# Kernel tuning notes

Measured on AMD Instinct MI355X. Metric: run time of the kernel, lower is better.

Reference implementation:

```python
import jax, jax.numpy as jnp
import numpy as np

NOISE_EPS = 1e-2   # Shazeer noisy-gating stddev floor
LN_EPS = 1e-6
LOSS_COEF = 0.01
K = 2              # num_activated_experts


def _layer_norm(x, w, b):
    mu = jnp.mean(x, axis=-1, keepdims=True)
    var = jnp.var(x, axis=-1, keepdims=True)
    return (x - mu) * jax.lax.rsqrt(var + LN_EPS) * w + b


def _cv_squared(v):
    return jnp.var(v) / (jnp.mean(v) ** 2 + 1e-10)


def _normal_cdf(z):
    return 0.5 * (1.0 + jax.scipy.special.erf(z / jnp.sqrt(jnp.asarray(2.0, z.dtype))))


def setup_inputs() -> dict:
    key = jax.random.key(0)
    ks = jax.random.split(key, 8)
    N, D, H, O, E = 8192, 512, 1024, 512, 8
    x = jax.random.normal(ks[0], (N, D), jnp.float32)
    x_offsets = jnp.sort(jax.random.randint(ks[1], (17,), 0, N)).astype(jnp.int64)
    noise = jax.random.normal(ks[2], (N, E), jnp.float32)
    s = 0.02
    return {
        "x": x,
        "x_offsets": x_offsets,
        "max_seq_len": 2048,
        "noise": noise,
        "norm_w": jnp.ones((D,), jnp.float32),
        "norm_bias": jnp.zeros((D,), jnp.float32),
        "w_gate": jax.random.normal(ks[3], (D, E), jnp.float32) * s,
        "w_noise": jax.random.normal(ks[4], (D, E), jnp.float32) * s,
        "W1": jax.random.normal(ks[5], (E, H, D), jnp.float32) * s,  # [E, model_d, input]
        "b1": jnp.zeros((E, H), jnp.float32),
        "W2": jax.random.normal(ks[6], (E, O, H), jnp.float32) * s,  # [E, output, model_d]
        "b2": jnp.zeros((E, O), jnp.float32),
        "output_weight": jax.random.normal(ks[7], (D, O), jnp.float32) * s,
    }


def reference(x, x_offsets, max_seq_len, noise, norm_w, norm_bias, w_gate, w_noise,
              W1, b1, W2, b2, output_weight):
    N, D = x.shape
    E = w_gate.shape[1]
    k_plus = min(K + 1, E)

    # pre-norm
    x_norm = _layer_norm(x, norm_w, norm_bias)

    # noisy top-k gating (training path)
    clean_logits = x_norm @ w_gate                      # [N, E]
    noise_stddev = jax.nn.softplus(x_norm @ w_noise) + NOISE_EPS
    noisy_logits = clean_logits + noise * noise_stddev

    top_logits, top_indices = jax.lax.top_k(noisy_logits, k_plus)   # [N, k+1]
    top_k_logits = top_logits[:, :K]
    top_k_indices = top_indices[:, :K]
    top_k_gates = jax.nn.softmax(top_k_logits, axis=-1)             # [N, K]

    rows = jnp.arange(N)[:, None]
    gates = jnp.zeros((N, E), top_k_gates.dtype).at[rows, top_k_indices].set(top_k_gates)

    # load = prob each expert is in top-k under the gating noise (Shazeer)
    flat = top_logits.reshape(-1)
    pos_in = jnp.arange(N) * k_plus + K
    thr_in = flat[pos_in][:, None]          # (k+1)-th value: threshold if already in
    thr_out = flat[pos_in - 1][:, None]     # k-th value: threshold if currently out
    is_in = noisy_logits > thr_in
    prob_in = _normal_cdf((clean_logits - thr_in) / noise_stddev)
    prob_out = _normal_cdf((clean_logits - thr_out) / noise_stddev)
    load_probs = jnp.where(is_in, prob_in, prob_out)                # [N, E]

    loss = LOSS_COEF * (_cv_squared(gates.sum(0)) + _cv_squared(load_probs.sum(0)))

    # dispatch stats: tokens per expert
    lengths = jnp.zeros((E,), jnp.float32).at[top_k_indices.reshape(-1)].add(1.0)
    load = lengths / lengths.sum()

    # grouped expert MLP (dense one-hot combine; gates are 0 for unrouted experts)
    h = jnp.einsum('nd,ehd->neh', x_norm, W1) + b1                  # [N, E, H]
    a = jax.nn.silu(h)
    y_e = jnp.einsum('neh,eoh->neo', a, W2) + b2                    # [N, E, O]
    y_moe = jnp.einsum('ne,neo->no', gates, y_e)                    # [N, O]

    # shared expert: addmm(y, shared_x=x, output_weight)
    y = y_moe + x @ output_weight
    return y, loss, load
```

## Files before the change

kernel.cpp:

```cpp
#include <hip/hip_runtime.h>
#include <math.h>

typedef unsigned short u16;
typedef unsigned int u32;

#define N_ROWS 8192
#define DDIM 512
#define HDIM 1024
#define ODIM 512
#define NEXP 8
#define MAXPAIRS (N_ROWS * 2)
#define MAXPOS (MAXPAIRS + NEXP * 128)
#define MAXTILES (MAXPOS / 128)

#define SM_CNT 0
#define SM_CUR 8
#define SM_AOFF 16
#define SM_GSUM 32
#define SM_LSUM 40
#define SM_WORDS 64

using short8 = __attribute__((ext_vector_type(8))) short;
using float4v = __attribute__((ext_vector_type(4))) float;

__device__ __forceinline__ u16 f2bf(float f) {
    union { float f; u32 u; } v; v.f = f;
    u32 u = v.u;
    return (u16)((u + 0x7fffu + ((u >> 16) & 1u)) >> 16);
}

__device__ __forceinline__ void async_copy16(u16* lds, const u16* g) {
    __builtin_amdgcn_global_load_lds(
        (const __attribute__((address_space(1))) void*)g,
        (__attribute__((address_space(3))) void*)lds, 16, 0, 0);
}

__global__ __launch_bounds__(512) void init1_kernel(int* small, float* zeropage) {
    int i = threadIdx.x;
    if (i < SM_WORDS) small[i] = 0;
    zeropage[i] = 0.f;
}

#define W1CONV_BLOCKS 4096
#define GATE_BLOCKS 512
__global__ __launch_bounds__(256) void combo_kernel(
    const float* __restrict__ x, const float* __restrict__ noise,
    const float* __restrict__ norm_w, const float* __restrict__ norm_b,
    const float* __restrict__ w_gate, const float* __restrict__ w_noise,
    const float* __restrict__ W1, const float* __restrict__ ow,
    u16* __restrict__ xnorm_bf, u16* __restrict__ x_bf,
    int* __restrict__ pair_expert, float* __restrict__ pair_gate,
    u16* __restrict__ W1b, u16* __restrict__ owT,
    int* __restrict__ small, int* __restrict__ bucket_rows)
{
    __shared__ __align__(16) float sh[NEXP * DDIM * 2 + 64];
    int b = blockIdx.x, tid = threadIdx.x;

    if (b >= GATE_BLOCKS) {
        int cb = b - GATE_BLOCKS;
        if (cb < W1CONV_BLOCKS) {
            size_t i = (size_t)cb * 256 + tid;
            float4 v = ((const float4*)W1)[i];
            ushort4 o;
            o.x = f2bf(v.x); o.y = f2bf(v.y); o.z = f2bf(v.z); o.w = f2bf(v.w);
            ((ushort4*)W1b)[i] = o;
        } else if (cb < W1CONV_BLOCKS + 256) {
            float (*tile)[33] = (float(*)[33])sh;
            int t = cb - W1CONV_BLOCKS;
            int bx = (t & 15) * 32, by = (t >> 4) * 32;
            int tx = tid & 31, ty = tid >> 5;
            for (int r = ty; r < 32; r += 8) tile[r][tx] = ow[(size_t)(by + r) * ODIM + bx + tx];
            __syncthreads();
            for (int r = ty; r < 32; r += 8) owT[(size_t)(bx + r) * DDIM + by + tx] = f2bf(tile[tx][r]);
        } else {
            int i = (cb - W1CONV_BLOCKS - 256) * 256 + tid;
            if (i < MAXPOS) bucket_rows[i] = -1;
        }
        return;
    }

    float* wgT = sh;
    float* wnT = sh + NEXP * DDIM;
    float* blk_g = sh + 2 * NEXP * DDIM;
    float* blk_l = blk_g + NEXP;
    int* blk_c = (int*)(blk_l + NEXP);
    float* smf = (float*)small;

    for (int i = tid; i < NEXP * DDIM; i += 256) {
        int d = i >> 3, e = i & 7;
        wgT[e * DDIM + d] = w_gate[i];
        wnT[e * DDIM + d] = w_noise[i];
    }
    if (tid < NEXP) { blk_g[tid] = 0.f; blk_l[tid] = 0.f; blk_c[tid] = 0; }
    __syncthreads();

    int wave = tid >> 6, lane = tid & 63;
    float nw[8], nb[8];
#pragma unroll
    for (int j = 0; j < 8; j++) { nw[j] = norm_w[j * 64 + lane]; nb[j] = norm_b[j * 64 + lane]; }

    for (int r = 0; r < 4; ++r) {
        int row = b * 16 + wave * 4 + r;
        const float* xr = x + (size_t)row * DDIM;
        float xv[8], s = 0.f, s2 = 0.f;
#pragma unroll
        for (int j = 0; j < 8; j++) { float v = xr[j * 64 + lane]; xv[j] = v; s += v; s2 += v * v; }
#pragma unroll
        for (int o = 32; o; o >>= 1) { s += __shfl_xor(s, o, 64); s2 += __shfl_xor(s2, o, 64); }
        float mu = s * (1.f / DDIM);
        float var = s2 * (1.f / DDIM) - mu * mu;
        float rstd = rsqrtf(var + 1e-6f);

        float acc[16];
#pragma unroll
        for (int e = 0; e < 16; e++) acc[e] = 0.f;
#pragma unroll
        for (int j = 0; j < 8; j++) {
            float v = (xv[j] - mu) * rstd * nw[j] + nb[j];
            int d = j * 64 + lane;
            xnorm_bf[(size_t)row * DDIM + d] = f2bf(v);
            x_bf[(size_t)row * DDIM + d] = f2bf(xv[j]);
#pragma unroll
            for (int e = 0; e < 8; e++) {
                acc[e] += v * wgT[e * DDIM + d];
                acc[8 + e] += v * wnT[e * DDIM + d];
            }
        }
#pragma unroll
        for (int e = 0; e < 16; e++)
#pragma unroll
            for (int o = 32; o; o >>= 1) acc[e] += __shfl_xor(acc[e], o, 64);

        float cl[8], sd[8], nz[8];
#pragma unroll
        for (int e = 0; e < 8; e++) {
            cl[e] = acc[e];
            float t = acc[8 + e];
            float sp = fmaxf(t, 0.f) + log1pf(expf(-fabsf(t)));
            sd[e] = sp + 0.01f;
            nz[e] = cl[e] + noise[(size_t)row * NEXP + e] * sd[e];
        }
        int idx[3]; float val[3]; u32 msk = 0;
#pragma unroll
        for (int t = 0; t < 3; t++) {
            float best = -INFINITY; int bi = 0;
#pragma unroll
            for (int e = 0; e < 8; e++)
                if (!((msk >> e) & 1) && nz[e] > best) { best = nz[e]; bi = e; }
            idx[t] = bi; val[t] = best; msk |= 1u << bi;
        }
        float e1 = expf(val[1] - val[0]);
        float g0 = 1.f / (1.f + e1), g1 = e1 / (1.f + e1);
        float thr_in = val[2], thr_out = val[1];

        if (lane == 0) {
            pair_expert[row * 2] = idx[0]; pair_gate[row * 2] = g0;
            pair_expert[row * 2 + 1] = idx[1]; pair_gate[row * 2 + 1] = g1;
            atomicAdd(&blk_g[idx[0]], g0); atomicAdd(&blk_g[idx[1]], g1);
            atomicAdd(&blk_c[idx[0]], 1); atomicAdd(&blk_c[idx[1]], 1);
#pragma unroll
            for (int e = 0; e < 8; e++) {
                float thr = (nz[e] > thr_in) ? thr_in : thr_out;
                float z = (cl[e] - thr) / sd[e];
                float p = 0.5f * (1.f + erff(z * 0.70710678118654752f));
                atomicAdd(&blk_l[e], p);
            }
        }
    }
    __syncthreads();
    if (tid < NEXP) {
        atomicAdd(smf + SM_GSUM + tid, blk_g[tid]);
        atomicAdd(smf + SM_LSUM + tid, blk_l[tid]);
        atomicAdd(&small[SM_CNT + tid], blk_c[tid]);
    }
}

__global__ __launch_bounds__(256) void scatter_kernel(
    const int* __restrict__ pair_expert, const float* __restrict__ pair_gate,
    int* __restrict__ small, int* __restrict__ bucket_rows, float* __restrict__ gate_by_pos,
    float* __restrict__ out_loss, float* __restrict__ out_load)
{
    __shared__ int aoff[NEXP + 1];
    __shared__ int blk_cnt[NEXP];
    __shared__ int blk_base[NEXP];
    int tid = threadIdx.x;
    if (tid == 0) {
        int acc = 0; aoff[0] = 0;
        for (int e = 0; e < NEXP; e++) { acc += (small[SM_CNT + e] + 127) & ~127; aoff[e + 1] = acc; }
    }
    if (tid < NEXP) blk_cnt[tid] = 0;
    __syncthreads();
    int p = blockIdx.x * 256 + tid;
    int e = pair_expert[p];
    int local = atomicAdd(&blk_cnt[e], 1);
    __syncthreads();
    if (tid < NEXP)
        blk_base[tid] = aoff[tid] + atomicAdd(&small[SM_CUR + tid], blk_cnt[tid]);
    if (blockIdx.x == 0 && tid < NEXP + 1) small[SM_AOFF + tid] = aoff[tid];
    __syncthreads();
    int pos = blk_base[e] + local;
    bucket_rows[pos] = p >> 1;
    gate_by_pos[pos] = pair_gate[p];

    if (blockIdx.x == 0 && tid == 0) {
        const float* gs = (const float*)small + SM_GSUM;
        const float* ls = (const float*)small + SM_LSUM;
        float cv[2];
        for (int t = 0; t < 2; t++) {
            const float* v = t ? ls : gs;
            float m = 0.f;
            for (int k = 0; k < NEXP; k++) m += v[k];
            m *= (1.f / NEXP);
            float var = 0.f;
            for (int k = 0; k < NEXP; k++) { float d = v[k] - m; var += d * d; }
            var *= (1.f / NEXP);
            cv[t] = var / (m * m + 1e-10f);
        }
        out_loss[0] = 0.01f * (cv[0] + cv[1]);
        int tot = 0;
        for (int k = 0; k < NEXP; k++) tot += small[SM_CNT + k];
        float inv = 1.f / (float)tot;
        for (int k = 0; k < NEXP; k++) out_load[k] = (float)small[SM_CNT + k] * inv;
    }
}


__global__ __launch_bounds__(256) void gemmA_kernel(
    const u16* __restrict__ xnorm, const u16* __restrict__ xbf,
    const u16* __restrict__ W1b, const u16* __restrict__ owT,
    const float* __restrict__ W2, u16* __restrict__ W2b,
    const int* __restrict__ bucket_rows, const int* __restrict__ small,
    const float* __restrict__ b1, const u16* __restrict__ zeropage,
    u16* __restrict__ a_buf, float* __restrict__ y)
{
    constexpr int KD = 512;
    __shared__ __align__(16) u16 As[128 * 64];
    __shared__ __align__(16) u16 Bs[128 * 64];

    int tid = threadIdx.x;
    if (blockIdx.y >= 10) {
        int j = (blockIdx.y - 10) * 136 + blockIdx.x;
        if (j >= 2048) return;
        size_t i = (size_t)j * 512 + tid;
#pragma unroll
        for (int t = 0; t < 2; t++, i += 256) {
            float4 v = ((const float4*)W2)[i];
            ushort4 o;
            o.x = f2bf(v.x); o.y = f2bf(v.y); o.z = f2bf(v.z); o.w = f2bf(v.w);
            ((ushort4*)W2b)[i] = o;
        }
        return;
    }

    bool m0 = blockIdx.y < 8;
    int base, bn, e = 0;
    const u16* Bsel;
    if (m0) {
        base = blockIdx.x * 128;
        if (base >= small[SM_AOFF + 8]) return;
        while (e < 7 && base >= small[SM_AOFF + e + 1]) ++e;
        bn = blockIdx.y * 128;
        Bsel = W1b + (size_t)e * HDIM * KD;
    } else {
        int j = (blockIdx.y - 8) * 136 + blockIdx.x;
        if (j >= 256) return;
        base = (j >> 2) * 128;
        bn = (j & 3) * 128;
        Bsel = owT;
    }

    int wave = tid >> 6, lane = tid & 63;
    int lr = lane >> 3;
    int lc = ((lane & 7) ^ lr) * 8;

    const u16* ga[4]; const u16* gb[4];
    u16* la[4]; u16* lb[4];
#pragma unroll
    for (int c = 0; c < 4; c++) {
        int tr = wave * 32 + c * 8;
        if (m0) {
            int r0 = bucket_rows[base + tr + lr];
            ga[c] = ((r0 < 0) ? zeropage : xnorm + (size_t)r0 * KD) + lc;
        } else {
            ga[c] = xbf + (size_t)(base + tr + lr) * KD + lc;
        }
        gb[c] = Bsel + (size_t)(bn + tr + lr) * KD + lc;
        la[c] = &As[tr * 64];
        lb[c] = &Bs[tr * 64];
    }

    int wm = (wave & 1) * 64, wn = (wave >> 1) * 64;
    int fr = lane & 15, kq = lane >> 4, f7 = fr & 7;

    float4v acc[4][4];
#pragma unroll
    for (int i = 0; i < 4; i++)
#pragma unroll
        for (int j = 0; j < 4; j++) acc[i][j] = (float4v){0.f, 0.f, 0.f, 0.f};

    for (int k0 = 0; k0 < KD; k0 += 64) {
        __syncthreads();
#pragma unroll
        for (int c = 0; c < 4; c++) async_copy16(la[c], ga[c] + k0);
#pragma unroll
        for (int c = 0; c < 4; c++) async_copy16(lb[c], gb[c] + k0);
        __syncthreads();
        short8 af[4][2], bf[4][2];
#pragma unroll
        for (int mt = 0; mt < 4; mt++)
#pragma unroll
            for (int kh = 0; kh < 2; kh++)
                af[mt][kh] = *(const short8*)&As[(wm + mt * 16 + fr) * 64 + (((kq + 4 * kh) ^ f7) * 8)];
#pragma unroll
        for (int nt = 0; nt < 4; nt++)
#pragma unroll
            for (int kh = 0; kh < 2; kh++)
                bf[nt][kh] = *(const short8*)&Bs[(wn + nt * 16 + fr) * 64 + (((kq + 4 * kh) ^ f7) * 8)];
#pragma unroll
        for (int mt = 0; mt < 4; mt++)
#pragma unroll
            for (int nt = 0; nt < 4; nt++) {
                acc[mt][nt] = __builtin_amdgcn_mfma_f32_16x16x32_bf16(af[mt][0], bf[nt][0], acc[mt][nt], 0, 0, 0);
                acc[mt][nt] = __builtin_amdgcn_mfma_f32_16x16x32_bf16(af[mt][1], bf[nt][1], acc[mt][nt], 0, 0, 0);
            }
    }

    int rbase = (lane >> 4) * 4, c16 = lane & 15;
#pragma unroll
    for (int nt = 0; nt < 4; nt++) {
        int gn = bn + wn + nt * 16 + c16;
        float bv = m0 ? b1[e * HDIM + gn] : 0.f;
#pragma unroll
        for (int mt = 0; mt < 4; mt++) {
            int gm = base + wm + mt * 16 + rbase;
#pragma unroll
            for (int r = 0; r < 4; r++) {
                float v = acc[mt][nt][r];
                if (m0) {
                    float h = v + bv;
                    float a = h * __builtin_amdgcn_rcpf(1.f + __expf(-h));
                    a_buf[(size_t)(gm + r) * HDIM + gn] = f2bf(a);
                } else {
                    y[(size_t)(gm + r) * ODIM + gn] = v;
                }
            }
        }
    }
}

__global__ __launch_bounds__(256) void gemmB_kernel(
    const u16* __restrict__ a_buf, const u16* __restrict__ W2b,
    const int* __restrict__ bucket_rows, const int* __restrict__ small,
    const float* __restrict__ b2, const float* __restrict__ gate_by_pos,
    float* __restrict__ y)
{
    constexpr int KD = 1024;
    __shared__ __align__(16) u16 As[128 * 32];
    __shared__ __align__(16) u16 Bs[128 * 32];

    int tid = threadIdx.x;
    int base = blockIdx.x * 128;
    if (base >= small[SM_AOFF + 8]) return;
    int e = 0;
    while (e < 7 && base >= small[SM_AOFF + e + 1]) ++e;
    int bn = blockIdx.y * 128;

    int wave = tid >> 6, lane = tid & 63;
    const int trow = wave * 32 + (lane >> 2);
    const int kcol = (lane & 3) * 8;
    const u16* ga0 = a_buf + (size_t)(base + trow) * KD + kcol;
    const u16* ga1 = a_buf + (size_t)(base + trow + 16) * KD + kcol;
    const u16* Bsel = W2b + (size_t)e * ODIM * KD;
    const u16* gb0 = Bsel + (size_t)(bn + trow) * KD + kcol;
    const u16* gb1 = Bsel + (size_t)(bn + trow + 16) * KD + kcol;
    u16* lA0 = &As[(wave * 32) * 32];
    u16* lA1 = &As[(wave * 32 + 16) * 32];
    u16* lB0 = &Bs[(wave * 32) * 32];
    u16* lB1 = &Bs[(wave * 32 + 16) * 32];

    int wm = (wave & 1) * 64, wn = (wave >> 1) * 64;
    int fr = lane & 15, kg = (lane >> 4) * 8;

    float4v acc[4][4];
#pragma unroll
    for (int i = 0; i < 4; i++)
#pragma unroll
        for (int j = 0; j < 4; j++) acc[i][j] = (float4v){0.f, 0.f, 0.f, 0.f};

    for (int k0 = 0; k0 < KD; k0 += 32) {
        __syncthreads();
        async_copy16(lA0, ga0 + k0);
        async_copy16(lA1, ga1 + k0);
        async_copy16(lB0, gb0 + k0);
        async_copy16(lB1, gb1 + k0);
        __syncthreads();
        short8 af[4], bf[4];
#pragma unroll
        for (int mt = 0; mt < 4; mt++) af[mt] = *(const short8*)&As[(wm + mt * 16 + fr) * 32 + kg];
#pragma unroll
        for (int nt = 0; nt < 4; nt++) bf[nt] = *(const short8*)&Bs[(wn + nt * 16 + fr) * 32 + kg];
#pragma unroll
        for (int mt = 0; mt < 4; mt++)
#pragma unroll
            for (int nt = 0; nt < 4; nt++)
                acc[mt][nt] = __builtin_amdgcn_mfma_f32_16x16x32_bf16(af[mt], bf[nt], acc[mt][nt], 0, 0, 0);
    }

    int rbase = (lane >> 4) * 4, c16 = lane & 15;
#pragma unroll
    for (int mt = 0; mt < 4; mt++) {
        int pos0 = base + wm + mt * 16 + rbase;
        int rows[4]; float gs[4];
#pragma unroll
        for (int r = 0; r < 4; r++) { rows[r] = bucket_rows[pos0 + r]; gs[r] = gate_by_pos[pos0 + r]; }
#pragma unroll
        for (int nt = 0; nt < 4; nt++) {
            int gn = bn + wn + nt * 16 + c16;
            float b2v = b2[e * ODIM + gn];
#pragma unroll
            for (int r = 0; r < 4; r++) {
                if (rows[r] >= 0)
                    unsafeAtomicAdd(&y[(size_t)rows[r] * ODIM + gn], gs[r] * (acc[mt][nt][r] + b2v));
            }
        }
    }
}

extern "C" void kernel_launch(void* const* d_in, const int* in_sizes, int n_in,
                              void* d_out, int out_size, void* d_ws, size_t ws_size,
                              hipStream_t stream)
{
    (void)in_sizes; (void)n_in; (void)out_size; (void)ws_size;
    const float* x = (const float*)d_in[0];
    const float* noise = (const float*)d_in[3];
    const float* norm_w = (const float*)d_in[4];
    const float* norm_b = (const float*)d_in[5];
    const float* w_gate = (const float*)d_in[6];
    const float* w_noise = (const float*)d_in[7];
    const float* W1 = (const float*)d_in[8];
    const float* b1 = (const float*)d_in[9];
    const float* W2 = (const float*)d_in[10];
    const float* b2 = (const float*)d_in[11];
    const float* ow = (const float*)d_in[12];

    float* y = (float*)d_out;
    float* out_loss = y + (size_t)N_ROWS * ODIM;
    float* out_load = out_loss + 1;

    char* ws = (char*)d_ws;
    size_t off = 0;
    auto alloc = [&](size_t b) { size_t p = off; off = (off + b + 255) & ~(size_t)255; return p; };
    u16* xnorm_bf = (u16*)(ws + alloc((size_t)N_ROWS * DDIM * 2));
    u16* x_bf     = (u16*)(ws + alloc((size_t)N_ROWS * DDIM * 2));
    u16* W1b      = (u16*)(ws + alloc((size_t)NEXP * HDIM * DDIM * 2));
    u16* W2b      = (u16*)(ws + alloc((size_t)NEXP * ODIM * HDIM * 2));
    u16* owT      = (u16*)(ws + alloc((size_t)DDIM * ODIM * 2));
    u16* a_buf    = (u16*)(ws + alloc((size_t)MAXPOS * HDIM * 2));
    int* pair_expert = (int*)(ws + alloc((size_t)MAXPAIRS * 4));
    float* pair_gate = (float*)(ws + alloc((size_t)MAXPAIRS * 4));
    float* gate_by_pos = (float*)(ws + alloc((size_t)MAXPOS * 4));
    int* bucket_rows = (int*)(ws + alloc((size_t)MAXPOS * 4));
    int* small       = (int*)(ws + alloc(SM_WORDS * 4));
    float* zeropage  = (float*)(ws + alloc(2048));

    init1_kernel<<<1, 512, 0, stream>>>(small, zeropage);
    combo_kernel<<<GATE_BLOCKS + W1CONV_BLOCKS + 256 + 68, 256, 0, stream>>>(
        x, noise, norm_w, norm_b, w_gate, w_noise, W1, ow,
        xnorm_bf, x_bf, pair_expert, pair_gate, W1b, owT, small, bucket_rows);
    scatter_kernel<<<MAXPAIRS / 256, 256, 0, stream>>>(pair_expert, pair_gate, small,
                                                       bucket_rows, gate_by_pos, out_loss, out_load);
    gemmA_kernel<<<dim3(MAXTILES, 10 + 16), 256, 0, stream>>>(xnorm_bf, x_bf, W1b, owT, W2, W2b,
                                                              bucket_rows, small, b1,
                                                              (const u16*)zeropage, a_buf, y);
    gemmB_kernel<<<dim3(MAXTILES, ODIM / 128), 256, 0, stream>>>(a_buf, W2b, bucket_rows, small,
                                                                 b2, gate_by_pos, y);
}
```

Before: 256.2 us.

## Move shared-expert GEMM from gemmA into gemmB with atomic accumulation

The shared-expert x@output_weight GEMM moves out of gemmA and into gemmB as extra blocks. y is now zeroed by new blocks in combo_kernel, and the shared GEMM adds into y atomically instead of storing directly. The aim is to shorten gemmA, which sits on the critical path before gemmB, and let the shared GEMM overlap with the expert down-projection. In exchange it adds a zero-fill pass over y and atomic adds for the shared output, and gemmB now uses the smaller 32-wide K tile for that GEMM.

```diff
diff --git a/kernel.cpp b/kernel.cpp
--- a/kernel.cpp
+++ b/kernel.cpp
@@ -43,6 +43,9 @@
 
 #define W1CONV_BLOCKS 4096
 #define GATE_BLOCKS 512
+#define OWT_BLOCKS 256
+#define BUCKET_BLOCKS 68
+#define YZERO_BLOCKS 1024
 __global__ __launch_bounds__(256) void combo_kernel(
     const float* __restrict__ x, const float* __restrict__ noise,
     const float* __restrict__ norm_w, const float* __restrict__ norm_b,
@@ -51,7 +54,7 @@
     u16* __restrict__ xnorm_bf, u16* __restrict__ x_bf,
     int* __restrict__ pair_expert, float* __restrict__ pair_gate,
     u16* __restrict__ W1b, u16* __restrict__ owT,
-    int* __restrict__ small, int* __restrict__ bucket_rows)
+    int* __restrict__ small, int* __restrict__ bucket_rows, float* __restrict__ y)
 {
     __shared__ __align__(16) float sh[NEXP * DDIM * 2 + 64];
     int b = blockIdx.x, tid = threadIdx.x;
@@ -64,7 +67,7 @@
             ushort4 o;
             o.x = f2bf(v.x); o.y = f2bf(v.y); o.z = f2bf(v.z); o.w = f2bf(v.w);
             ((ushort4*)W1b)[i] = o;
-        } else if (cb < W1CONV_BLOCKS + 256) {
+        } else if (cb < W1CONV_BLOCKS + OWT_BLOCKS) {
             float (*tile)[33] = (float(*)[33])sh;
             int t = cb - W1CONV_BLOCKS;
             int bx = (t & 15) * 32, by = (t >> 4) * 32;
@@ -72,9 +75,15 @@
             for (int r = ty; r < 32; r += 8) tile[r][tx] = ow[(size_t)(by + r) * ODIM + bx + tx];
             __syncthreads();
             for (int r = ty; r < 32; r += 8) owT[(size_t)(bx + r) * DDIM + by + tx] = f2bf(tile[tx][r]);
+        } else if (cb < W1CONV_BLOCKS + OWT_BLOCKS + BUCKET_BLOCKS) {
+            int i = (cb - W1CONV_BLOCKS - OWT_BLOCKS) * 256 + tid;
+            if (i < MAXPOS) bucket_rows[i] = -1;
         } else {
-            int i = (cb - W1CONV_BLOCKS - 256) * 256 + tid;
-            if (i < MAXPOS) bucket_rows[i] = -1;
+            int zb = cb - W1CONV_BLOCKS - OWT_BLOCKS - BUCKET_BLOCKS;
+            size_t i = (size_t)zb * 1024 + tid;
+            float4 zero = {0.f, 0.f, 0.f, 0.f};
+#pragma unroll
+            for (int t = 0; t < 4; t++, i += 256) ((float4*)y)[i] = zero;
         }
         return;
     }
@@ -224,22 +233,20 @@
     }
 }
 
-
 __global__ __launch_bounds__(256) void gemmA_kernel(
-    const u16* __restrict__ xnorm, const u16* __restrict__ xbf,
-    const u16* __restrict__ W1b, const u16* __restrict__ owT,
+    const u16* __restrict__ xnorm, const u16* __restrict__ W1b,
     const float* __restrict__ W2, u16* __restrict__ W2b,
     const int* __restrict__ bucket_rows, const int* __restrict__ small,
     const float* __restrict__ b1, const u16* __restrict__ zeropage,
-    u16* __restrict__ a_buf, float* __restrict__ y)
+    u16* __restrict__ a_buf)
 {
     constexpr int KD = 512;
     __shared__ __align__(16) u16 As[128 * 64];
     __shared__ __align__(16) u16 Bs[128 * 64];
 
     int tid = threadIdx.x;
-    if (blockIdx.y >= 10) {
-        int j = (blockIdx.y - 10) * 136 + blockIdx.x;
+    if (blockIdx.y >= 8) {
+        int j = (blockIdx.y - 8) * 136 + blockIdx.x;
         if (j >= 2048) return;
         size_t i = (size_t)j * 512 + tid;
 #pragma unroll
@@ -252,134 +259,129 @@
         return;
     }
 
-    bool m0 = blockIdx.y < 8;
-    int base, bn, e = 0;
-    const u16* Bsel;
-    if (m0) {
-        base = blockIdx.x * 128;
-        if (base >= small[SM_AOFF + 8]) return;
-        while (e < 7 && base >= small[SM_AOFF + e + 1]) ++e;
-        bn = blockIdx.y * 128;
-        Bsel = W1b + (size_t)e * HDIM * KD;
-    } else {
-        int j = (blockIdx.y - 8) * 136 + blockIdx.x;
-        if (j >= 256) return;
-        base = (j >> 2) * 128;
-        bn = (j & 3) * 128;
-        Bsel = owT;
-    }
-
-    int wave = tid >> 6, lane = tid & 63;
-    int lr = lane >> 3;
-    int lc = ((lane & 7) ^ lr) * 8;
-
-    const u16* ga[4]; const u16* gb[4];
-    u16* la[4]; u16* lb[4];
-#pragma unroll
-    for (int c = 0; c < 4; c++) {
-        int tr = wave * 32 + c * 8;
-        if (m0) {
-            int r0 = bucket_rows[base + tr + lr];
-            ga[c] = ((r0 < 0) ? zeropage : xnorm + (size_t)r0 * KD) + lc;
-        } else {
-            ga[c] = xbf + (size_t)(base + tr + lr) * KD + lc;
-        }
-        gb[c] = Bsel + (size_t)(bn + tr + lr) * KD + lc;
-        la[c] = &As[tr * 64];
-        lb[c] = &Bs[tr * 64];
-    }
-
-    int wm = (wave & 1) * 64, wn = (wave >> 1) * 64;
-    int fr = lane & 15, kq = lane >> 4, f7 = fr & 7;
-
-    float4v acc[4][4];
-#pragma unroll
-    for (int i = 0; i < 4; i++)
-#pragma unroll
-        for (int j = 0; j < 4; j++) acc[i][j] = (float4v){0.f, 0.f, 0.f, 0.f};
-
-    for (int k0 = 0; k0 < KD; k0 += 64) {
-        __syncthreads();
-#pragma unroll
-        for (int c = 0; c < 4; c++) async_copy16(la[c], ga[c] + k0);
-#pragma unroll
-        for (int c = 0; c < 4; c++) async_copy16(lb[c], gb[c] + k0);
-        __syncthreads();
-        short8 af[4][2], bf[4][2];
-#pragma unroll
-        for (int mt = 0; mt < 4; mt++)
-#pragma unroll
-            for (int kh = 0; kh < 2; kh++)
-                af[mt][kh] = *(const short8*)&As[(wm + mt * 16 + fr) * 64 + (((kq + 4 * kh) ^ f7) * 8)];
-#pragma unroll
-        for (int nt = 0; nt < 4; nt++)
-#pragma unroll
-            for (int kh = 0; kh < 2; kh++)
-                bf[nt][kh] = *(const short8*)&Bs[(wn + nt * 16 + fr) * 64 + (((kq + 4 * kh) ^ f7) * 8)];
-#pragma unroll
-        for (int mt = 0; mt < 4; mt++)
-#pragma unroll
-            for (int nt = 0; nt < 4; nt++) {
-                acc[mt][nt] = __builtin_amdgcn_mfma_f32_16x16x32_bf16(af[mt][0], bf[nt][0], acc[mt][nt], 0, 0, 0);
-                acc[mt][nt] = __builtin_amdgcn_mfma_f32_16x16x32_bf16(af[mt][1], bf[nt][1], acc[mt][nt], 0, 0, 0);
-            }
-    }
-
-    int rbase = (lane >> 4) * 4, c16 = lane & 15;
-#pragma unroll
-    for (int nt = 0; nt < 4; nt++) {
-        int gn = bn + wn + nt * 16 + c16;
-        float bv = m0 ? b1[e * HDIM + gn] : 0.f;
-#pragma unroll
-        for (int mt = 0; mt < 4; mt++) {
-            int gm = base + wm + mt * 16 + rbase;
-#pragma unroll
-            for (int r = 0; r < 4; r++) {
-                float v = acc[mt][nt][r];
-                if (m0) {
-                    float h = v + bv;
-                    float a = h * __builtin_amdgcn_rcpf(1.f + __expf(-h));
-                    a_buf[(size_t)(gm + r) * HDIM + gn] = f2bf(a);
-                } else {
-                    y[(size_t)(gm + r) * ODIM + gn] = v;
-                }
-            }
-        }
-    }
-}
-
-__global__ __launch_bounds__(256) void gemmB_kernel(
-    const u16* __restrict__ a_buf, const u16* __restrict__ W2b,
-    const int* __restrict__ bucket_rows, const int* __restrict__ small,
-    const float* __restrict__ b2, const float* __restrict__ gate_by_pos,
-    float* __restrict__ y)
-{
-    constexpr int KD = 1024;
-    __shared__ __align__(16) u16 As[128 * 32];
-    __shared__ __align__(16) u16 Bs[128 * 32];
-
-    int tid = threadIdx.x;
     int base = blockIdx.x * 128;
     if (base >= small[SM_AOFF + 8]) return;
     int e = 0;
     while (e < 7 && base >= small[SM_AOFF + e + 1]) ++e;
     int bn = blockIdx.y * 128;
-
+    const u16* Bsel = W1b + (size_t)e * HDIM * KD;
+
+    int wave = tid >> 6, lane = tid & 63;
+    int lr = lane >> 3;
+    int lc = ((lane & 7) ^ lr) * 8;
+
+    const u16* ga[4]; const u16* gb[4];
+    u16* la[4]; u16* lb[4];
+#pragma unroll
+    for (int c = 0; c < 4; c++) {
+        int tr = wave * 32 + c * 8;
+        int r0 = bucket_rows[base + tr + lr];
+        ga[c] = ((r0 < 0) ? zeropage : xnorm + (size_t)r0 * KD) + lc;
+        gb[c] = Bsel + (size_t)(bn + tr + lr) * KD + lc;
+        la[c] = &As[tr * 64];
+        lb[c] = &Bs[tr * 64];
+    }
+
+    int wm = (wave & 1) * 64, wn = (wave >> 1) * 64;
+    int fr = lane & 15, kq = lane >> 4, f7 = fr & 7;
+
+    float4v acc[4][4];
+#pragma unroll
+    for (int i = 0; i < 4; i++)
+#pragma unroll
+        for (int j = 0; j < 4; j++) acc[i][j] = (float4v){0.f, 0.f, 0.f, 0.f};
+
+    for (int k0 = 0; k0 < KD; k0 += 64) {
+        __syncthreads();
+#pragma unroll
+        for (int c = 0; c < 4; c++) async_copy16(la[c], ga[c] + k0);
+#pragma unroll
+        for (int c = 0; c < 4; c++) async_copy16(lb[c], gb[c] + k0);
+        __syncthreads();
+        short8 af[4][2], bf[4][2];
+#pragma unroll
+        for (int mt = 0; mt < 4; mt++)
+#pragma unroll
+            for (int kh = 0; kh < 2; kh++)
+                af[mt][kh] = *(const short8*)&As[(wm + mt * 16 + fr) * 64 + (((kq + 4 * kh) ^ f7) * 8)];
+#pragma unroll
+        for (int nt = 0; nt < 4; nt++)
+#pragma unroll
+            for (int kh = 0; kh < 2; kh++)
+                bf[nt][kh] = *(const short8*)&Bs[(wn + nt * 16 + fr) * 64 + (((kq + 4 * kh) ^ f7) * 8)];
+#pragma unroll
+        for (int mt = 0; mt < 4; mt++)
+#pragma unroll
+            for (int nt = 0; nt < 4; nt++) {
+                acc[mt][nt] = __builtin_amdgcn_mfma_f32_16x16x32_bf16(af[mt][0], bf[nt][0], acc[mt][nt], 0, 0, 0);
+                acc[mt][nt] = __builtin_amdgcn_mfma_f32_16x16x32_bf16(af[mt][1], bf[nt][1], acc[mt][nt], 0, 0, 0);
+            }
+    }
+
+    int rbase = (lane >> 4) * 4, c16 = lane & 15;
+#pragma unroll
+    for (int nt = 0; nt < 4; nt++) {
+        int gn = bn + wn + nt * 16 + c16;
+        float bv = b1[e * HDIM + gn];
+#pragma unroll
+        for (int mt = 0; mt < 4; mt++) {
+            int gm = base + wm + mt * 16 + rbase;
+#pragma unroll
+            for (int r = 0; r < 4; r++) {
+                float h = acc[mt][nt][r] + bv;
+                float a = h * __builtin_amdgcn_rcpf(1.f + __expf(-h));
+                a_buf[(size_t)(gm + r) * HDIM + gn] = f2bf(a);
+            }
+        }
+    }
+}
+
+__global__ __launch_bounds__(256) void gemmB_kernel(
+    const u16* __restrict__ a_buf, const u16* __restrict__ W2b,
+    const u16* __restrict__ xbf, const u16* __restrict__ owT,
+    const int* __restrict__ bucket_rows, const int* __restrict__ small,
+    const float* __restrict__ b2, const float* __restrict__ gate_by_pos,
+    float* __restrict__ y)
+{
+    __shared__ __align__(16) u16 As[128 * 32];
+    __shared__ __align__(16) u16 Bs[128 * 32];
+
+    int tid = threadIdx.x;
     int wave = tid >> 6, lane = tid & 63;
     const int trow = wave * 32 + (lane >> 2);
     const int kcol = (lane & 3) * 8;
-    const u16* ga0 = a_buf + (size_t)(base + trow) * KD + kcol;
-    const u16* ga1 = a_buf + (size_t)(base + trow + 16) * KD + kcol;
-    const u16* Bsel = W2b + (size_t)e * ODIM * KD;
-    const u16* gb0 = Bsel + (size_t)(bn + trow) * KD + kcol;
-    const u16* gb1 = Bsel + (size_t)(bn + trow + 16) * KD + kcol;
+    int wm = (wave & 1) * 64, wn = (wave >> 1) * 64;
+    int fr = lane & 15, kg = (lane >> 4) * 8;
+
+    bool expertPath = blockIdx.y < 4;
+    int base, bn, e = 0, KD;
+    const u16 *ga0, *ga1, *gb0, *gb1;
+    if (expertPath) {
+        KD = 1024;
+        base = blockIdx.x * 128;
+        if (base >= small[SM_AOFF + 8]) return;
+        while (e < 7 && base >= small[SM_AOFF + e + 1]) ++e;
+        bn = blockIdx.y * 128;
+        ga0 = a_buf + (size_t)(base + trow) * KD + kcol;
+        ga1 = a_buf + (size_t)(base + trow + 16) * KD + kcol;
+        const u16* Bsel = W2b + (size_t)e * ODIM * KD;
+        gb0 = Bsel + (size_t)(bn + trow) * KD + kcol;
+        gb1 = Bsel + (size_t)(bn + trow + 16) * KD + kcol;
+    } else {
+        KD = 512;
+        int j = (blockIdx.y - 4) * 136 + blockIdx.x;
+        if (j >= 256) return;
+        base = (j >> 2) * 128;
+        bn = (j & 3) * 128;
+        ga0 = xbf + (size_t)(base + trow) * KD + kcol;
+        ga1 = xbf + (size_t)(base + trow + 16) * KD + kcol;
+        gb0 = owT + (size_t)(bn + trow) * KD + kcol;
+        gb1 = owT + (size_t)(bn + trow + 16) * KD + kcol;
+    }
     u16* lA0 = &As[(wave * 32) * 32];
     u16* lA1 = &As[(wave * 32 + 16) * 32];
     u16* lB0 = &Bs[(wave * 32) * 32];
     u16* lB1 = &Bs[(wave * 32 + 16) * 32];
-
-    int wm = (wave & 1) * 64, wn = (wave >> 1) * 64;
-    int fr = lane & 15, kg = (lane >> 4) * 8;
 
     float4v acc[4][4];
 #pragma unroll
@@ -407,20 +409,34 @@
     }
 
     int rbase = (lane >> 4) * 4, c16 = lane & 15;
-#pragma unroll
-    for (int mt = 0; mt < 4; mt++) {
-        int pos0 = base + wm + mt * 16 + rbase;
-        int rows[4]; float gs[4];
-#pragma unroll
-        for (int r = 0; r < 4; r++) { rows[r] = bucket_rows[pos0 + r]; gs[r] = gate_by_pos[pos0 + r]; }
-#pragma unroll
-        for (int nt = 0; nt < 4; nt++) {
-            int gn = bn + wn + nt * 16 + c16;
-            float b2v = b2[e * ODIM + gn];
-#pragma unroll
-            for (int r = 0; r < 4; r++) {
-                if (rows[r] >= 0)
-                    unsafeAtomicAdd(&y[(size_t)rows[r] * ODIM + gn], gs[r] * (acc[mt][nt][r] + b2v));
+    if (expertPath) {
+#pragma unroll
+        for (int mt = 0; mt < 4; mt++) {
+            int pos0 = base + wm + mt * 16 + rbase;
+            int rows[4]; float gs[4];
+#pragma unroll
+            for (int r = 0; r < 4; r++) { rows[r] = bucket_rows[pos0 + r]; gs[r] = gate_by_pos[pos0 + r]; }
+#pragma unroll
+            for (int nt = 0; nt < 4; nt++) {
+                int gn = bn + wn + nt * 16 + c16;
+                float b2v = b2[e * ODIM + gn];
+#pragma unroll
+                for (int r = 0; r < 4; r++) {
+                    if (rows[r] >= 0)
+                        unsafeAtomicAdd(&y[(size_t)rows[r] * ODIM + gn], gs[r] * (acc[mt][nt][r] + b2v));
+                }
+            }
+        }
+    } else {
+#pragma unroll
+        for (int mt = 0; mt < 4; mt++) {
+            int gm = base + wm + mt * 16 + rbase;
+#pragma unroll
+            for (int nt = 0; nt < 4; nt++) {
+                int gn = bn + wn + nt * 16 + c16;
+#pragma unroll
+                for (int r = 0; r < 4; r++)
+                    unsafeAtomicAdd(&y[(size_t)(gm + r) * ODIM + gn], acc[mt][nt][r]);
             }
         }
     }
@@ -464,14 +480,15 @@
     float* zeropage  = (float*)(ws + alloc(2048));
 
     init1_kernel<<<1, 512, 0, stream>>>(small, zeropage);
-    combo_kernel<<<GATE_BLOCKS + W1CONV_BLOCKS + 256 + 68, 256, 0, stream>>>(
+    combo_kernel<<<GATE_BLOCKS + W1CONV_BLOCKS + OWT_BLOCKS + BUCKET_BLOCKS + YZERO_BLOCKS,
+                   256, 0, stream>>>(
         x, noise, norm_w, norm_b, w_gate, w_noise, W1, ow,
-        xnorm_bf, x_bf, pair_expert, pair_gate, W1b, owT, small, bucket_rows);
+        xnorm_bf, x_bf, pair_expert, pair_gate, W1b, owT, small, bucket_rows, y);
     scatter_kernel<<<MAXPAIRS / 256, 256, 0, stream>>>(pair_expert, pair_gate, small,
                                                        bucket_rows, gate_by_pos, out_loss, out_load);
-    gemmA_kernel<<<dim3(MAXTILES, 10 + 16), 256, 0, stream>>>(xnorm_bf, x_bf, W1b, owT, W2, W2b,
-                                                              bucket_rows, small, b1,
-                                                              (const u16*)zeropage, a_buf, y);
-    gemmB_kernel<<<dim3(MAXTILES, ODIM / 128), 256, 0, stream>>>(a_buf, W2b, bucket_rows, small,
-                                                                 b2, gate_by_pos, y);
-}
+    gemmA_kernel<<<dim3(MAXTILES, 8 + 16), 256, 0, stream>>>(xnorm_bf, W1b, W2, W2b,
+                                                             bucket_rows, small, b1,
+                                                             (const u16*)zeropage, a_buf);
+    gemmB_kernel<<<dim3(MAXTILES, 6), 256, 0, stream>>>(a_buf, W2b, x_bf, owT, bucket_rows,
+                                                        small, b2, gate_by_pos, y);
+}
```

Measured after the change: 254.9 us. Within noise of the previous version (-0.5%).
